# Performance work log

Measured on AMD Instinct MI355X. Metric: run time of the kernel, lower is better.

## Reference

```python
import jax, jax.numpy as jnp
import numpy as np
from jax import lax

B, L, E, P, K, KS, H, T = 64, 512, 256, 64, 512, 3, 512, 53
V, MAXL = 50000, 512


def _span_idx(k):
    ks, kl = jax.random.split(k)
    starts = jax.random.randint(ks, (B,), 1, L - 9)
    spans = jax.random.randint(kl, (B,), 0, 8)
    return jnp.stack([starts, starts + spans], axis=1)  # [B,2], 1<=s<=e<L-1


def setup_inputs() -> dict:
    key = jax.random.key(0)
    ks = jax.random.split(key, 12)
    context = jax.random.randint(ks[0], (B, L), 0, V)
    subject_idx = _span_idx(ks[1])
    object_idx = _span_idx(ks[2])
    subject_dis = jax.random.randint(ks[3], (B, L), 0, 2 * MAXL)
    object_dis = jax.random.randint(ks[4], (B, L), 0, 2 * MAXL)
    embed_table = jax.random.normal(ks[5], (V, E), jnp.float32) * 0.02
    pos_table = jax.random.normal(ks[6], (2 * MAXL, P), jnp.float32) * 0.02
    Cin = 3 * E + 2 * P
    conv_w = jax.random.normal(ks[7], (K, Cin, KS), jnp.float32) * 0.02
    conv_b = jnp.zeros((K,), jnp.float32)
    lin1_w = jax.random.normal(ks[8], (H, K), jnp.float32) * 0.02
    lin1_b = jnp.zeros((H,), jnp.float32)
    lin2_w = jax.random.normal(ks[9], (T, 6 * E + H), jnp.float32) * 0.02
    lin2_b = jnp.zeros((T,), jnp.float32)
    return {"context": context, "subject_idx": subject_idx, "object_idx": object_idx,
            "subject_dis": subject_dis, "object_dis": object_dis,
            "embed_table": embed_table, "pos_table": pos_table,
            "conv_w": conv_w, "conv_b": conv_b,
            "lin1_w": lin1_w, "lin1_b": lin1_b, "lin2_w": lin2_w, "lin2_b": lin2_b}


def _entity_features(embed, idx):
    # embed: [B,L,E'], idx: [B,2] (start,end) inclusive span
    s, e = idx[:, 0], idx[:, 1]
    pos = jnp.arange(L)
    mask = (pos[None, :] >= s[:, None]) & (pos[None, :] <= e[:, None])  # [B,L]
    cnt = mask.sum(axis=1).astype(embed.dtype)[:, None]
    mean = jnp.einsum('ble,bl->be', embed, mask.astype(embed.dtype)) / cnt
    bidx = jnp.arange(embed.shape[0])
    left = embed[bidx, s - 1]                       # start>=1 always in data (torch: start>=0 branch)
    right_ok = (e + 1) < L
    right = jnp.where(right_ok[:, None], embed[bidx, jnp.clip(e + 1, 0, L - 1)], 0.0)
    return jnp.concatenate([mean, left, right], axis=1)  # [B,3E']


def reference(context, subject_idx, object_idx, subject_dis, object_dis,
              embed_table, pos_table, conv_w, conv_b,
              lin1_w, lin1_b, lin2_w, lin2_b):
    embed = embed_table[context]                    # [B,L,E]
    subj = _entity_features(embed, subject_idx)     # [B,3E]
    obj = _entity_features(embed, object_idx)       # [B,3E]

    # shift-and-concat window features (zero pad one step each side)
    epad = jnp.pad(embed, ((0, 0), (1, 1), (0, 0)))
    word = jnp.concatenate([epad[:, :-2], epad[:, 1:-1], epad[:, 2:]], axis=2)  # [B,L,3E]

    pos_feat = jnp.concatenate([pos_table[subject_dis], pos_table[object_dis]], axis=2)  # [B,L,2P]
    sent = jnp.concatenate([word, pos_feat], axis=2).transpose(0, 2, 1)  # [B,C,L]

    conv = lax.conv_general_dilated(sent, conv_w, window_strides=(1,),
                                    padding=[(KS // 2, KS // 2)],
                                    dimension_numbers=('NCH', 'OIH', 'NCH'))
    conv = conv + conv_b[None, :, None]             # [B,K,L]
    pooled = conv.max(axis=2)                       # global maxpool -> [B,K]
    sent_h = jnp.tanh(pooled @ lin1_w.T + lin1_b)   # [B,H]

    com = jnp.concatenate([subj, obj, sent_h], axis=1)  # [B,6E+H]
    scores = com @ lin2_w.T + lin2_b                # [B,T]; decode = argmax(scores, 1)
    return scores
```

## Files before the change

kernel.cpp:

```cpp
#include <hip/hip_runtime.h>
#include <hip/hip_bf16.h>
#include <hip/hip_fp8.h>
#include <stdint.h>

#define B_   64
#define L_   512
#define E_   256
#define P_   64
#define KOUT 512
#define KS_  3
#define H_   512
#define T_   53
#define CINW 2688
#define LE   516
#define LPP  514
#define COMW 2048

#define FP8_S    64.0f
#define DESCALE  (1.0f / 4096.0f)

#define SEC_CW    0
#define SEC_EMBP  512
#define SEC_POSP  (SEC_EMBP + (B_ * LE / 4))
#define SEC_ENT   (SEC_POSP + (B_ * LPP / 4))
#define SEC_POOL  (SEC_ENT + 2 * B_)
#define SEC_END   (SEC_POOL + 32)

typedef __attribute__((ext_vector_type(4))) float f32x4;

__device__ __forceinline__ unsigned enc_f(float x) {
    unsigned u = __float_as_uint(x);
    return (u & 0x80000000u) ? ~u : (u | 0x80000000u);
}
__device__ __forceinline__ float dec_f(unsigned e) {
    return __uint_as_float((e & 0x80000000u) ? (e & 0x7fffffffu) : ~e);
}
__device__ __forceinline__ unsigned char f8c(float x) {
    __hip_fp8_e4m3 t(x);
    return t.__x;
}

__device__ __forceinline__ void cp16(const void* g, void* l) {
    __builtin_amdgcn_global_load_lds(
        (const __attribute__((address_space(1))) unsigned int*)g,
        (__attribute__((address_space(3))) unsigned int*)l,
        16, 0, 0);
}

__global__ void prep(const float* __restrict__ conv_w,
                     const int* __restrict__ context,
                     const int* __restrict__ sidx,
                     const int* __restrict__ oidx,
                     const int* __restrict__ sdis,
                     const int* __restrict__ odis,
                     const float* __restrict__ etab,
                     const float* __restrict__ ptab,
                     unsigned char* __restrict__ wce,
                     unsigned char* __restrict__ wcp,
                     __hip_bfloat16* __restrict__ wcorr,
                     unsigned char* __restrict__ embp,
                     unsigned char* __restrict__ posp,
                     float* __restrict__ com,
                     unsigned* __restrict__ pooled) {
    __shared__ float w[CINW];
    const int blk = blockIdx.x;
    const int tid = threadIdx.x;

    if (blk < SEC_EMBP) {
        int n = blk;
        const float* src = conv_w + (size_t)n * CINW;
        for (int i = tid; i < CINW; i += 256) w[i] = src[i];
        __syncthreads();
        for (int i = tid; i < 5 * E_; i += 256) {
            int d = i >> 8, c = i & 255;
            float s = 0.f;
#pragma unroll
            for (int tau = 0; tau <= 2; tau++) {
                int seg = d - tau;
                if (seg >= 0 && seg <= 2) s += w[(seg * 256 + c) * 3 + tau];
            }
            wce[((size_t)d * KOUT + n) * E_ + c] = f8c(s * FP8_S);
        }
        for (int i = tid; i < 3 * 128; i += 256) {
            int tau = i >> 7, p = i & 127;
            wcp[((size_t)tau * KOUT + n) * 128 + p] = f8c(w[(768 + p) * 3 + tau] * FP8_S);
        }
        for (int i = tid; i < 2 * E_; i += 256) {
            int which = i >> 8, c = i & 255;
            wcorr[((size_t)which * KOUT + n) * E_ + c] =
                __float2bfloat16(which ? w[c * 3 + 2] : w[(512 + c) * 3 + 0]);
        }
    } else if (blk < SEC_POSP) {
        int row = (blk - SEC_EMBP) * 4 + (tid >> 6);
        int lane = tid & 63;
        int b = row / LE, r = row % LE;
        unsigned char* out = embp + (size_t)row * E_;
        if (r < 2 || r >= LE - 2) {
            *(uchar4*)(out + lane * 4) = (uchar4){0, 0, 0, 0};
            return;
        }
        int token = context[b * L_ + (r - 2)];
        float4 v = *(const float4*)(etab + (size_t)token * E_ + lane * 4);
        uchar4 pk;
        pk.x = f8c(v.x * FP8_S); pk.y = f8c(v.y * FP8_S);
        pk.z = f8c(v.z * FP8_S); pk.w = f8c(v.w * FP8_S);
        *(uchar4*)(out + lane * 4) = pk;
    } else if (blk < SEC_ENT) {
        int row = (blk - SEC_POSP) * 4 + (tid >> 6);
        int lane = tid & 63;
        int b = row / LPP, r = row % LPP;
        unsigned char* out = posp + (size_t)row * 128;
        if (r < 1 || r >= LPP - 1) {
            *(unsigned short*)(out + lane * 2) = 0;
            return;
        }
        int l = r - 1;
        int which = lane >> 5;
        int i2 = (lane & 31) * 2;
        int t = which ? odis[b * L_ + l] : sdis[b * L_ + l];
        float2 v = *(const float2*)(ptab + (size_t)t * P_ + i2);
        unsigned short pk = (unsigned short)f8c(v.x * FP8_S)
                          | ((unsigned short)f8c(v.y * FP8_S) << 8);
        *(unsigned short*)(out + which * 64 + i2) = pk;
    } else if (blk < SEC_POOL) {
        int idx = blk - SEC_ENT;
        int b = idx >> 1, which = idx & 1;
        const int* sp = which ? oidx : sidx;
        int s = sp[b * 2 + 0], e = sp[b * 2 + 1];
        const int* ctx = context + b * L_;
        float* outb = com + (size_t)b * COMW + which * 768;
        int d = tid;
        float sum = 0.f;
        for (int x = s; x <= e; ++x) sum += etab[(size_t)ctx[x] * E_ + d];
        outb[d] = sum / (float)(e - s + 1);
        outb[256 + d] = etab[(size_t)ctx[s - 1] * E_ + d];
        float r = 0.f;
        if (e + 1 < L_) r = etab[(size_t)ctx[e + 1] * E_ + d];
        outb[512 + d] = r;
    } else {
        int base = ((blk - SEC_POOL) * 256 + tid) * 4;
        *(uint4*)(pooled + base) = (uint4){0, 0, 0, 0};
    }
}

__global__ void corr_k(const int* __restrict__ ctx,
                       const float* __restrict__ etab,
                       const __hip_bfloat16* __restrict__ wcorr,
                       float* __restrict__ corr) {
    int wid = blockIdx.x * 4 + (threadIdx.x >> 6);
    int lane = threadIdx.x & 63;
    int n4    = wid & 127;
    int which = (wid >> 7) & 1;
    int b     = wid >> 8;
    int token = ctx[b * L_ + (which ? L_ - 1 : 0)];
    float4 ev = *(const float4*)(etab + (size_t)token * E_ + lane * 4);
#pragma unroll
    for (int k = 0; k < 4; k++) {
        int n = n4 * 4 + k;
        const __hip_bfloat16* wr = wcorr + ((size_t)which * KOUT + n) * E_ + lane * 4;
        float s = ev.x * __bfloat162float(wr[0]) + ev.y * __bfloat162float(wr[1])
                + ev.z * __bfloat162float(wr[2]) + ev.w * __bfloat162float(wr[3]);
#pragma unroll
        for (int off = 32; off > 0; off >>= 1) s += __shfl_down(s, off, 64);
        if (lane == 0) corr[(b * 2 + which) * KOUT + n] = s;
    }
}

__global__ void conv_gemm_pool(const unsigned char* __restrict__ embp,
                               const unsigned char* __restrict__ posp,
                               const unsigned char* __restrict__ wce,
                               const unsigned char* __restrict__ wcp,
                               const float* __restrict__ corr,
                               unsigned* __restrict__ pooled) {
    __shared__ unsigned char sA[128 * 64];
    __shared__ unsigned char sB[128 * 64];

    const int tid  = threadIdx.x;
    const int wave = tid >> 6;
    const int lane = tid & 63;
    const int mt = blockIdx.x;
    const int nt = blockIdx.y;
    const int b  = mt >> 2;
    const int l0 = (mt & 3) * 128;
    const int n0 = nt * 128;

    const int wr = (wave & 1) * 64;
    const int wc = (wave >> 1) * 64;
    const int m  = lane & 15;
    const int q  = lane >> 4;

    f32x4 acc[4][4];
#pragma unroll
    for (int i = 0; i < 4; i++)
#pragma unroll
        for (int j = 0; j < 4; j++) acc[i][j] = (f32x4){0.f, 0.f, 0.f, 0.f};

    const int rowA = tid >> 2;
    const int cswz = ((tid & 3) ^ ((tid >> 3) & 3)) * 16;

    auto step = [&](const char* Ab, int AsB, const char* Bb, int BsB) {
        cp16(Ab + rowA * AsB + cswz, (char*)sA + tid * 16);
        cp16(Bb + rowA * BsB + cswz, (char*)sB + tid * 16);
        cp16(Ab + (rowA + 64) * AsB + cswz, (char*)sA + (tid + 256) * 16);
        cp16(Bb + (rowA + 64) * BsB + cswz, (char*)sB + (tid + 256) * 16);
        __syncthreads();
#pragma unroll
        for (int h = 0; h < 2; h++) {
            long af[4], bfr[4];
#pragma unroll
            for (int i = 0; i < 4; i++) {
                int row = wr + i * 16 + m;
                int pc = ((h << 1) | (q >> 1)) ^ ((row >> 1) & 3);
                af[i] = *(const long*)((const char*)sA + row * 64 + pc * 16 + (q & 1) * 8);
            }
#pragma unroll
            for (int j = 0; j < 4; j++) {
                int row = wc + j * 16 + m;
                int pc = ((h << 1) | (q >> 1)) ^ ((row >> 1) & 3);
                bfr[j] = *(const long*)((const char*)sB + row * 64 + pc * 16 + (q & 1) * 8);
            }
#pragma unroll
            for (int i = 0; i < 4; i++)
#pragma unroll
                for (int j = 0; j < 4; j++)
                    acc[i][j] = __builtin_amdgcn_mfma_f32_16x16x32_fp8_fp8(
                        af[i], bfr[j], acc[i][j], 0, 0, 0);
        }
        __syncthreads();
    };

    for (int t = 0; t < 5; t++) {
        const char* Abase = (const char*)(embp + (size_t)(b * LE + l0 + t) * E_);
        const char* Bbase = (const char*)(wce + (size_t)(t * KOUT + n0) * E_);
        for (int kc = 0; kc < E_; kc += 64)
            step(Abase + kc, E_, Bbase + kc, E_);
    }
    for (int t = 0; t < 3; t++) {
        const char* Abase = (const char*)(posp + (size_t)(b * LPP + l0 + t) * 128);
        const char* Bbase = (const char*)(wcp + (size_t)(t * KOUT + n0) * 128);
        for (int kc = 0; kc < 128; kc += 64)
            step(Abase + kc, 128, Bbase + kc, 128);
    }

    const float* corrb = corr + b * 2 * KOUT;
#pragma unroll
    for (int j = 0; j < 4; j++) {
        int col = n0 + wc + j * 16 + m;
        float mx = -3.4e38f;
#pragma unroll
        for (int i = 0; i < 4; i++)
#pragma unroll
            for (int r = 0; r < 4; r++) {
                float v = acc[i][j][r] * DESCALE;
                int l = l0 + wr + i * 16 + q * 4 + r;
                if (l == 0)      v -= corrb[col];
                if (l == L_ - 1) v -= corrb[KOUT + col];
                mx = fmaxf(mx, v);
            }
        mx = fmaxf(mx, __shfl_xor(mx, 16, 64));
        mx = fmaxf(mx, __shfl_xor(mx, 32, 64));
        if (q == 0) atomicMax(&pooled[b * KOUT + col], enc_f(mx));
    }
}

__global__ void lin1_k(const unsigned* __restrict__ pooled,
                       const float* __restrict__ conv_b,
                       const float* __restrict__ lin1_w,
                       const float* __restrict__ lin1_b,
                       float* __restrict__ com) {
    int bid = blockIdx.x;
    int wave = threadIdx.x >> 6, lane = threadIdx.x & 63;
    int b = bid >> 7;
    int h = (bid & 127) * 4 + wave;
    const float* w = lin1_w + (size_t)h * KOUT;
    const unsigned* pb = pooled + b * KOUT;
    float s = 0.f;
#pragma unroll
    for (int i = 0; i < 8; i++) {
        int k = lane + 64 * i;
        s += (dec_f(pb[k]) + conv_b[k]) * w[k];
    }
#pragma unroll
    for (int off = 32; off > 0; off >>= 1) s += __shfl_down(s, off, 64);
    if (lane == 0) com[(size_t)b * COMW + 1536 + h] = tanhf(s + lin1_b[h]);
}

__global__ void lin2_k(const float* __restrict__ com,
                       const float* __restrict__ lin2_w,
                       const float* __restrict__ lin2_b,
                       float* __restrict__ out) {
    int b = blockIdx.x;
    int wave = threadIdx.x >> 6, lane = threadIdx.x & 63;
    int t = blockIdx.y * 4 + wave;
    if (t >= T_) return;
    const float* w = lin2_w + (size_t)t * COMW;
    const float* c = com + (size_t)b * COMW;
    float s = 0.f;
#pragma unroll
    for (int i = 0; i < 32; i++) {
        int k = lane + 64 * i;
        s += c[k] * w[k];
    }
#pragma unroll
    for (int off = 32; off > 0; off >>= 1) s += __shfl_down(s, off, 64);
    if (lane == 0) out[b * T_ + t] = s + lin2_b[t];
}

extern "C" void kernel_launch(void* const* d_in, const int* in_sizes, int n_in,
                              void* d_out, int out_size, void* d_ws, size_t ws_size,
                              hipStream_t stream) {
    const int*   context = (const int*)d_in[0];
    const int*   sidx    = (const int*)d_in[1];
    const int*   oidx    = (const int*)d_in[2];
    const int*   sdis    = (const int*)d_in[3];
    const int*   odis    = (const int*)d_in[4];
    const float* etab    = (const float*)d_in[5];
    const float* ptab    = (const float*)d_in[6];
    const float* conv_w  = (const float*)d_in[7];
    const float* conv_b  = (const float*)d_in[8];
    const float* lin1_w  = (const float*)d_in[9];
    const float* lin1_b  = (const float*)d_in[10];
    const float* lin2_w  = (const float*)d_in[11];
    const float* lin2_b  = (const float*)d_in[12];
    float* out = (float*)d_out;

    char* ws = (char*)d_ws;
    size_t off = 0;
    unsigned char* embp = (unsigned char*)(ws + off);
    off += (size_t)B_ * LE * E_;
    off = (off + 255) & ~(size_t)255;
    unsigned char* posp = (unsigned char*)(ws + off);
    off += (size_t)B_ * LPP * 128;
    off = (off + 255) & ~(size_t)255;
    unsigned char* wce = (unsigned char*)(ws + off);
    off += (size_t)5 * KOUT * E_;
    off = (off + 255) & ~(size_t)255;
    unsigned char* wcp = (unsigned char*)(ws + off);
    off += (size_t)3 * KOUT * 128;
    off = (off + 255) & ~(size_t)255;
    __hip_bfloat16* wcorr = (__hip_bfloat16*)(ws + off);
    off += (size_t)2 * KOUT * E_ * 2;
    off = (off + 255) & ~(size_t)255;
    float* corr = (float*)(ws + off);
    off += (size_t)B_ * 2 * KOUT * 4;
    off = (off + 255) & ~(size_t)255;
    unsigned* pooled = (unsigned*)(ws + off);
    off += (size_t)B_ * KOUT * 4;
    off = (off + 255) & ~(size_t)255;
    float* com = (float*)(ws + off);
    off += (size_t)B_ * COMW * 4;

    prep<<<dim3(SEC_END), dim3(256), 0, stream>>>(
        conv_w, context, sidx, oidx, sdis, odis, etab, ptab,
        wce, wcp, wcorr, embp, posp, com, pooled);
    corr_k<<<dim3(4096), dim3(256), 0, stream>>>(context, etab, wcorr, corr);
    conv_gemm_pool<<<dim3(256, 4), dim3(256), 0, stream>>>(embp, posp, wce, wcp, corr, pooled);
    lin1_k<<<dim3(8192), dim3(256), 0, stream>>>(pooled, conv_b, lin1_w, lin1_b, com);
    lin2_k<<<dim3(B_, 14), dim3(256), 0, stream>>>(com, lin2_w, lin2_b, out);
}
```

Baseline: 189.0 us.

## Use 16x16x128 scaled FP8 MFMA with double-buffered 128-wide K tiles

Replaces the 16x16x32 fp8 MFMA loop, which staged 64-byte K chunks, with the gfx950 scaled MFMA 16x16x128 over 128-byte K tiles. These are double-buffered in LDS, and the next tile's global_load_lds is issued before computing the current one, with a vmcnt wait. The intent is fewer MFMA issues and fewer barriers per K step, plus overlap of global loads with compute. In exchange LDS use grows to 64KB per block, and launch_bounds(256,2) may limit register use.

After: 181.4 us. 4.0% less time.

```diff
diff --git a/kernel.cpp b/kernel.cpp
--- a/kernel.cpp
+++ b/kernel.cpp
@@ -27,6 +27,8 @@
 #define SEC_END   (SEC_POOL + 32)
 
 typedef __attribute__((ext_vector_type(4))) float f32x4;
+typedef __attribute__((ext_vector_type(4))) int   i32x4;
+typedef __attribute__((ext_vector_type(8))) int   i32x8;
 
 __device__ __forceinline__ unsigned enc_f(float x) {
     unsigned u = __float_as_uint(x);
@@ -166,18 +168,18 @@
     }
 }
 
-__global__ void conv_gemm_pool(const unsigned char* __restrict__ embp,
-                               const unsigned char* __restrict__ posp,
-                               const unsigned char* __restrict__ wce,
-                               const unsigned char* __restrict__ wcp,
-                               const float* __restrict__ corr,
-                               unsigned* __restrict__ pooled) {
-    __shared__ unsigned char sA[128 * 64];
-    __shared__ unsigned char sB[128 * 64];
+__global__ void __launch_bounds__(256, 2)
+conv_gemm_pool(const unsigned char* __restrict__ embp,
+               const unsigned char* __restrict__ posp,
+               const unsigned char* __restrict__ wce,
+               const unsigned char* __restrict__ wcp,
+               const float* __restrict__ corr,
+               unsigned* __restrict__ pooled) {
+    __shared__ unsigned char sT[2][2][128 * 128];
 
     const int tid  = threadIdx.x;
+    const int lane = tid & 63;
     const int wave = tid >> 6;
-    const int lane = tid & 63;
     const int mt = blockIdx.x;
     const int nt = blockIdx.y;
     const int b  = mt >> 2;
@@ -195,51 +197,82 @@
 #pragma unroll
         for (int j = 0; j < 4; j++) acc[i][j] = (f32x4){0.f, 0.f, 0.f, 0.f};
 
-    const int rowA = tid >> 2;
-    const int cswz = ((tid & 3) ^ ((tid >> 3) & 3)) * 16;
-
-    auto step = [&](const char* Ab, int AsB, const char* Bb, int BsB) {
-        cp16(Ab + rowA * AsB + cswz, (char*)sA + tid * 16);
-        cp16(Bb + rowA * BsB + cswz, (char*)sB + tid * 16);
-        cp16(Ab + (rowA + 64) * AsB + cswz, (char*)sA + (tid + 256) * 16);
-        cp16(Bb + (rowA + 64) * BsB + cswz, (char*)sB + (tid + 256) * 16);
-        __syncthreads();
-#pragma unroll
-        for (int h = 0; h < 2; h++) {
-            long af[4], bfr[4];
-#pragma unroll
-            for (int i = 0; i < 4; i++) {
-                int row = wr + i * 16 + m;
-                int pc = ((h << 1) | (q >> 1)) ^ ((row >> 1) & 3);
-                af[i] = *(const long*)((const char*)sA + row * 64 + pc * 16 + (q & 1) * 8);
-            }
-#pragma unroll
-            for (int j = 0; j < 4; j++) {
-                int row = wc + j * 16 + m;
-                int pc = ((h << 1) | (q >> 1)) ^ ((row >> 1) & 3);
-                bfr[j] = *(const long*)((const char*)sB + row * 64 + pc * 16 + (q & 1) * 8);
-            }
+    const int srow = tid >> 3;
+    const int ssw  = ((tid & 7) ^ (srow & 7)) << 4;
+
+    auto bases = [&](int t, const char*& A, int& As, const char*& Bx, int& Bs) {
+        if (t < 10) {
+            int tap = t >> 1, kc = (t & 1) << 7;
+            A  = (const char*)embp + ((size_t)(b * LE + l0 + tap) << 8) + kc;
+            As = E_;
+            Bx = (const char*)wce + ((size_t)(tap * KOUT + n0) << 8) + kc;
+            Bs = E_;
+        } else {
+            int tap = t - 10;
+            A  = (const char*)posp + ((size_t)(b * LPP + l0 + tap) << 7);
+            As = 128;
+            Bx = (const char*)wcp + ((size_t)(tap * KOUT + n0) << 7);
+            Bs = 128;
+        }
+    };
+
+    auto stage = [&](int bf_, const char* A, int As, const char* Bx, int Bs) {
+        char* dA = (char*)&sT[bf_][0][0] + tid * 16;
+        char* dB = (char*)&sT[bf_][1][0] + tid * 16;
+#pragma unroll
+        for (int rnd = 0; rnd < 4; rnd++) {
+            int r = srow + rnd * 32;
+            cp16(A  + r * As + ssw, dA + rnd * 4096);
+            cp16(Bx + r * Bs + ssw, dB + rnd * 4096);
+        }
+    };
+
+    auto frag = [&](const unsigned char* base, int row) -> i32x8 {
+        const unsigned char* rp = base + row * 128;
+        int x  = (row & 7) << 4;
+        i32x4 lo = *(const i32x4*)(rp + (((q << 1) << 4) ^ x));
+        i32x4 hi = *(const i32x4*)(rp + ((((q << 1) | 1) << 4) ^ x));
+        return (i32x8){lo[0], lo[1], lo[2], lo[3], hi[0], hi[1], hi[2], hi[3]};
+    };
+
+    auto compute = [&](int bf_) {
+        const unsigned char* pA = &sT[bf_][0][0];
+        const unsigned char* pB = &sT[bf_][1][0];
+        i32x8 af[4];
+#pragma unroll
+        for (int i = 0; i < 4; i++) af[i] = frag(pA, wr + i * 16 + m);
+#pragma unroll
+        for (int j = 0; j < 4; j++) {
+            i32x8 bfv = frag(pB, wc + j * 16 + m);
 #pragma unroll
             for (int i = 0; i < 4; i++)
-#pragma unroll
-                for (int j = 0; j < 4; j++)
-                    acc[i][j] = __builtin_amdgcn_mfma_f32_16x16x32_fp8_fp8(
-                        af[i], bfr[j], acc[i][j], 0, 0, 0);
-        }
-        __syncthreads();
+                acc[i][j] = __builtin_amdgcn_mfma_scale_f32_16x16x128_f8f6f4(
+                    af[i], bfv, acc[i][j], 0, 0, 0, 0x7f7f7f7f, 0, 0x7f7f7f7f);
+        }
     };
 
-    for (int t = 0; t < 5; t++) {
-        const char* Abase = (const char*)(embp + (size_t)(b * LE + l0 + t) * E_);
-        const char* Bbase = (const char*)(wce + (size_t)(t * KOUT + n0) * E_);
-        for (int kc = 0; kc < E_; kc += 64)
-            step(Abase + kc, E_, Bbase + kc, E_);
-    }
-    for (int t = 0; t < 3; t++) {
-        const char* Abase = (const char*)(posp + (size_t)(b * LPP + l0 + t) * 128);
-        const char* Bbase = (const char*)(wcp + (size_t)(t * KOUT + n0) * 128);
-        for (int kc = 0; kc < 128; kc += 64)
-            step(Abase + kc, 128, Bbase + kc, 128);
+    {
+        const char *A0, *B0; int As0, Bs0;
+        bases(0, A0, As0, B0, Bs0);
+        stage(0, A0, As0, B0, Bs0);
+    }
+    int cur = 0;
+#pragma unroll 1
+    for (int t = 0; t < 13; t++) {
+        if (t < 12) {
+            const char *A1, *B1; int As1, Bs1;
+            bases(t + 1, A1, As1, B1, Bs1);
+            stage(cur ^ 1, A1, As1, B1, Bs1);
+            asm volatile("s_waitcnt vmcnt(8)" ::: "memory");
+        } else {
+            asm volatile("s_waitcnt vmcnt(0)" ::: "memory");
+        }
+        __builtin_amdgcn_s_barrier();
+        __builtin_amdgcn_sched_barrier(0);
+        compute(cur);
+        __builtin_amdgcn_sched_barrier(0);
+        __builtin_amdgcn_s_barrier();
+        cur ^= 1;
     }
 
     const float* corrb = corr + b * 2 * KOUT;
```
